# Optimization experiments

Hardware: AMD Instinct MI355X
Metric: run time of the kernel (lower is better)

## Reference

```python
import jax, jax.numpy as jnp
import numpy as np

EPS = 1e-6


def setup_inputs() -> dict:
    key = jax.random.key(0)
    ks = jax.random.split(key, 8)
    B, L, C = 2, 512, 768  # d_model=768, C//3=256
    pairDim = 128
    inp = {
        "x": jax.random.normal(ks[0], (B, L, C), dtype=jnp.float32),
        "ln_w": jnp.ones((C,), jnp.float32),
        "ln_b": jnp.zeros((C,), jnp.float32),
        # torch Linear weights are [out, in]
        "W1": jax.random.normal(ks[1], (256, C // 3), jnp.float32) * (1.0 / np.sqrt(C // 3)),
        "b1": jax.random.normal(ks[2], (256,), jnp.float32) * 0.02,
        "Wa": jax.random.normal(ks[3], (64, 64), jnp.float32) * (1.0 / np.sqrt(64)),
        "ba": jax.random.normal(ks[4], (64,), jnp.float32) * 0.02,
        "W2": jax.random.normal(ks[5], (pairDim, 32), jnp.float32) * (1.0 / np.sqrt(32)),
        "b2": jax.random.normal(ks[6], (pairDim,), jnp.float32) * 0.02,
    }
    return inp


def _layernorm(x, w, b):
    mu = jnp.mean(x, axis=-1, keepdims=True)
    var = jnp.mean(jnp.square(x - mu), axis=-1, keepdims=True)
    return (x - mu) * jax.lax.rsqrt(var + EPS) * w + b


def reference(x, ln_w, ln_b, W1, b1, Wa, ba, W2, b2):
    B, L, C = x.shape
    h = _layernorm(x, ln_w, ln_b)                      # [B,L,C]
    h = h.reshape(B, L, 3, C // 3)                     # [B,L,3,C/3]
    t = (h @ W1.T + b1).reshape(B, L, 3, 32, 8)        # [B,L,3,32,8]
    # outer product t[...,i]*t[...,j] then mean over the 3 chunks (fused)
    mean_out = jnp.einsum('blkci,blkcj->blcij', t, t) / 3.0  # [B,L,32,8,8]
    mean_out = mean_out.reshape(B, L, 32, 64).transpose(0, 2, 1, 3)  # [B,32,L,64]
    mean_trans = jax.nn.gelu(mean_out @ Wa.T + ba, approximate=False)  # [B,32,L,64]
    raw = jnp.einsum('bcld,bcmd->bclm', mean_out, mean_trans)  # [B,32,L,L]
    raw = raw.transpose(0, 2, 3, 1)                    # [B,L,L,32]
    return raw @ W2.T + b2                             # [B,L,L,pairDim]
```

## Files before the change

### kernel.cpp

```cpp
#include <hip/hip_runtime.h>
#include <math.h>


typedef __attribute__((ext_vector_type(8))) _Float16 half8;
typedef __attribute__((ext_vector_type(4))) _Float16 half4;
typedef __attribute__((ext_vector_type(4))) float f32x4;

#define MFMA_F16(a,b,c) __builtin_amdgcn_mfma_f32_16x16x32_f16((a),(b),(c),0,0,0)

static __device__ inline unsigned pack2f16(float a, float b) {
    _Float16 ha = (_Float16)a, hb = (_Float16)b;
    unsigned short ua = __builtin_bit_cast(unsigned short, ha);
    unsigned short ub = __builtin_bit_cast(unsigned short, hb);
    return (unsigned)ua | ((unsigned)ub << 16);
}

static __device__ inline half8 cvt8(float4 u, float4 v) {
    half8 h;
    h[0] = (_Float16)u.x; h[1] = (_Float16)u.y; h[2] = (_Float16)u.z; h[3] = (_Float16)u.w;
    h[4] = (_Float16)v.x; h[5] = (_Float16)v.y; h[6] = (_Float16)v.z; h[7] = (_Float16)v.w;
    return h;
}

static __device__ inline float gelu_fast(float v) {
    float u  = 0.7978845608028654f * (v + 0.044715f * v * v * v);
    float t  = __expf(-2.0f * fabsf(u));
    float th = 1.0f - 2.0f * t / (1.0f + t);
    th = copysignf(th, u);
    return 0.5f * v * (1.0f + th);
}

__global__ __launch_bounds__(256) void k0_pack(const float* __restrict__ W1, _Float16* __restrict__ W1H)
{
    int flat8 = blockIdx.x * 256 + threadIdx.x;
    int j  = flat8 >> 5, i8 = flat8 & 31;
    int nt = j >> 4, lr = j & 15, ks = i8 >> 2, lk = i8 & 3;
    const float4* src = (const float4*)(W1 + (size_t)j * 256 + (size_t)i8 * 8);
    half8 h = cvt8(src[0], src[1]);
    *(half8*)(W1H + (((size_t)(nt * 8 + ks) * 64) + lk * 16 + lr) * 8) = h;
}

__global__ __launch_bounds__(256, 2) void k1_rowstage2(
    const float* __restrict__ x, const float* __restrict__ ln_w, const float* __restrict__ ln_b,
    const _Float16* __restrict__ W1H, const float* __restrict__ b1,
    const float* __restrict__ Wa, const float* __restrict__ ba,
    _Float16* __restrict__ mo_g, _Float16* __restrict__ mt_g)
{
    const int blk = blockIdx.x;
    const int b   = blk >> 8;
    const int l0  = (blk & 255) << 1;
    const int tid = threadIdx.x;
    const int w   = tid >> 6;
    const int lane = tid & 63;
    const int lr  = lane & 15;
    const int lk  = lane >> 4;

    __shared__ _Float16 hs16[16 * 280];
    __shared__ float ts2[2][776];
    __shared__ float mos2[2][2176];

    half8 bfr[32];
    #pragma unroll
    for (int ks = 0; ks < 8; ++ks)
        #pragma unroll
        for (int n = 0; n < 4; ++n)
            bfr[ks * 4 + n] = *(const half8*)(W1H + (((size_t)((w * 4 + n) * 8 + ks) * 64) + lane) * 8);

    half8 waf[2];
    #pragma unroll
    for (int ks = 0; ks < 2; ++ks) {
        const float* wp = Wa + (size_t)(w * 16 + lr) * 64 + ks * 32 + lk * 8;
        waf[ks] = cvt8(*(const float4*)wp, *(const float4*)(wp + 4));
    }
    const float4 baq = *(const float4*)(ba + w * 16 + lk * 4);

    if (w < 2) {
        const float4* xrow = (const float4*)(x + ((size_t)(b * 512 + l0 + w)) * 768);
        float4 xv[3];
        float s1 = 0.f, s2 = 0.f;
        #pragma unroll
        for (int e4 = 0; e4 < 3; ++e4) {
            float4 v = xrow[lane + 64 * e4];
            xv[e4] = v;
            s1 += v.x + v.y + v.z + v.w;
            s2 += v.x * v.x + v.y * v.y + v.z * v.z + v.w * v.w;
        }
        #pragma unroll
        for (int off = 32; off > 0; off >>= 1) {
            s1 += __shfl_xor(s1, off);
            s2 += __shfl_xor(s2, off);
        }
        float mu   = s1 * (1.0f / 768.0f);
        float var  = s2 * (1.0f / 768.0f) - mu * mu;
        float rstd = rsqrtf(var + 1e-6f);
        #pragma unroll
        for (int e4 = 0; e4 < 3; ++e4) {
            float4 lw = ((const float4*)ln_w)[lane + 64 * e4];
            float4 lb = ((const float4*)ln_b)[lane + 64 * e4];
            half4 h4;
            h4[0] = (_Float16)((xv[e4].x - mu) * rstd * lw.x + lb.x);
            h4[1] = (_Float16)((xv[e4].y - mu) * rstd * lw.y + lb.y);
            h4[2] = (_Float16)((xv[e4].z - mu) * rstd * lw.z + lb.z);
            h4[3] = (_Float16)((xv[e4].w - mu) * rstd * lw.w + lb.w);
            *(half4*)&hs16[(w * 3 + e4) * 280 + 4 * lane] = h4;
        }
    }
    __syncthreads();

    {
        f32x4 acc[4] = {};
        #pragma unroll
        for (int ks = 0; ks < 8; ++ks) {
            half8 af = *(const half8*)&hs16[lr * 280 + ks * 32 + lk * 8];
            #pragma unroll
            for (int n = 0; n < 4; ++n)
                acc[n] = MFMA_F16(af, bfr[ks * 4 + n], acc[n]);
        }
        #pragma unroll
        for (int n = 0; n < 4; ++n) {
            int j = (w * 4 + n) * 16 + lr;
            float bb = b1[j];
            #pragma unroll
            for (int jj = 0; jj < 4; ++jj) {
                int m = lk * 4 + jj;
                if (m < 6) {
                    int r = (m >= 3) ? 1 : 0, k = m - r * 3;
                    ts2[r][k * 256 + j] = acc[n][jj] + bb;
                }
            }
        }
    }
    __syncthreads();

    {
        const int c = tid >> 3, i = tid & 7;
        #pragma unroll
        for (int r = 0; r < 2; ++r) {
            float ti0 = ts2[r][c * 8 + i], ti1 = ts2[r][256 + c * 8 + i], ti2 = ts2[r][512 + c * 8 + i];
            float4 a0 = *(const float4*)&ts2[r][c * 8];
            float4 a1 = *(const float4*)&ts2[r][c * 8 + 4];
            float4 b0 = *(const float4*)&ts2[r][256 + c * 8];
            float4 b1v = *(const float4*)&ts2[r][256 + c * 8 + 4];
            float4 d0 = *(const float4*)&ts2[r][512 + c * 8];
            float4 d1 = *(const float4*)&ts2[r][512 + c * 8 + 4];
            float m0 = (ti0 * a0.x + ti1 * b0.x + ti2 * d0.x) * (1.0f / 3.0f);
            float m1 = (ti0 * a0.y + ti1 * b0.y + ti2 * d0.y) * (1.0f / 3.0f);
            float m2 = (ti0 * a0.z + ti1 * b0.z + ti2 * d0.z) * (1.0f / 3.0f);
            float m3 = (ti0 * a0.w + ti1 * b0.w + ti2 * d0.w) * (1.0f / 3.0f);
            float m4 = (ti0 * a1.x + ti1 * b1v.x + ti2 * d1.x) * (1.0f / 3.0f);
            float m5 = (ti0 * a1.y + ti1 * b1v.y + ti2 * d1.y) * (1.0f / 3.0f);
            float m6 = (ti0 * a1.z + ti1 * b1v.z + ti2 * d1.z) * (1.0f / 3.0f);
            float m7 = (ti0 * a1.w + ti1 * b1v.w + ti2 * d1.w) * (1.0f / 3.0f);
            *(float4*)&mos2[r][c * 68 + i * 8]     = make_float4(m0, m1, m2, m3);
            *(float4*)&mos2[r][c * 68 + i * 8 + 4] = make_float4(m4, m5, m6, m7);
            half8 h8;
            h8[0] = (_Float16)m0; h8[1] = (_Float16)m1; h8[2] = (_Float16)m2; h8[3] = (_Float16)m3;
            h8[4] = (_Float16)m4; h8[5] = (_Float16)m5; h8[6] = (_Float16)m6; h8[7] = (_Float16)m7;
            size_t mobase = ((size_t)(b * 32 + c) * 512 + (l0 + r)) * 64 + i * 8;
            *(half8*)(mo_g + mobase) = h8;
        }
    }
    __syncthreads();

    #pragma unroll
    for (int nt2 = 0; nt2 < 4; ++nt2) {
        const int r = nt2 >> 1, ch = nt2 & 1;
        f32x4 acc = { baq.x, baq.y, baq.z, baq.w };
        #pragma unroll
        for (int ks = 0; ks < 2; ++ks) {
            const float* mp = &mos2[r][(ch * 16 + lr) * 68 + ks * 32 + lk * 8];
            half8 mof = cvt8(*(const float4*)mp, *(const float4*)(mp + 4));
            acc = MFMA_F16(waf[ks], mof, acc);
        }
        half4 o;
        #pragma unroll
        for (int j = 0; j < 4; ++j)
            o[j] = (_Float16)gelu_fast(acc[j]);
        *(half4*)(mt_g + ((size_t)(b * 32 + ch * 16 + lr) * 512 + (l0 + r)) * 64 + w * 16 + lk * 4) = o;
    }
}

__global__ __launch_bounds__(256, 2) void k2_mfma(
    const _Float16* __restrict__ mo, const _Float16* __restrict__ mt,
    const float* __restrict__ W2, const float* __restrict__ b2,
    float* __restrict__ out)
{
    __shared__ _Float16 raw16[512 * 40];
    __shared__ float sc[4][2048];

    const int tid  = threadIdx.x;
    const int w    = tid >> 6;
    const int lane = tid & 63;
    const int lr   = lane & 15;
    const int lk   = lane >> 4;

    const int flat = blockIdx.x;
    const int nf   = (flat & 7) * 128 + (flat >> 3);
    const int m0   = (nf & 31) << 4;
    const int l0   = ((nf >> 5) & 15) << 5;
    const int b    = nf >> 9;

    #pragma unroll
    for (int cp = 0; cp < 4; ++cp) {
        const int c0 = w * 8 + cp * 2;
        f32x4 acc[2][2] = {};
        #pragma unroll
        for (int ci = 0; ci < 2; ++ci) {
            const int c = c0 + ci;
            const _Float16* mo_c = mo + (((size_t)(b * 32 + c) * 512) + l0) * 64;
            const _Float16* mt_c = mt + (((size_t)(b * 32 + c) * 512) + m0) * 64;
            #pragma unroll
            for (int ks = 0; ks < 2; ++ks) {
                half8 bfrag = *(const half8*)(mt_c + (size_t)lr * 64 + ks * 32 + lk * 8);
                #pragma unroll
                for (int rh = 0; rh < 2; ++rh) {
                    half8 afrag = *(const half8*)(mo_c + (size_t)(rh * 16 + lr) * 64 + ks * 32 + lk * 8);
                    acc[ci][rh] = MFMA_F16(afrag, bfrag, acc[ci][rh]);
                }
            }
        }
        #pragma unroll
        for (int rh = 0; rh < 2; ++rh) {
            #pragma unroll
            for (int j = 0; j < 4; ++j) {
                int pair = (rh * 16 + lk * 4 + j) * 16 + lr;
                int sw   = (((pair >> 3) & 1) << 3) | (((pair >> 6) & 1) << 4);
                *(unsigned*)&raw16[pair * 40 + (c0 ^ sw)] = pack2f16(acc[0][rh][j], acc[1][rh][j]);
            }
        }
    }

    half8 wfrag[8]; float4 b2q[8];
    #pragma unroll
    for (int c8 = 0; c8 < 8; ++c8) {
        const float* wp = W2 + (size_t)(c8 * 16 + lr) * 32 + lk * 8;
        wfrag[c8] = cvt8(*(const float4*)wp, *(const float4*)(wp + 4));
        b2q[c8]   = *(const float4*)(b2 + c8 * 16 + lk * 4);
    }
    __syncthreads();

    for (int i = 0; i < 8; ++i) {
        const int r  = w * 8 + i;
        const int pr = r * 16 + lr;
        const int swr = (((pr >> 3) & 1) << 3) | (((pr >> 6) & 1) << 4);
        half8 a = *(const half8*)&raw16[pr * 40 + ((lk * 8) ^ swr)];

        #pragma unroll
        for (int c8 = 0; c8 < 8; ++c8) {
            f32x4 d = { b2q[c8].x, b2q[c8].y, b2q[c8].z, b2q[c8].w };
            d = MFMA_F16(wfrag[c8], a, d);
            int chunk = (c8 * 4 + lk) ^ lr;
            *(f32x4*)&sc[w][lr * 128 + chunk * 4] = d;
        }
        float* ob = out + (((size_t)(b * 512 + l0 + r)) * 512 + m0) * 128;
        #pragma unroll
        for (int s = 0; s < 8; ++s) {
            int mm = s * 2 + (lane >> 5);
            int cp = (lane & 31) ^ mm;
            f32x4 v = *(const f32x4*)&sc[w][mm * 128 + cp * 4];
            __builtin_nontemporal_store(v, (f32x4*)(ob + s * 256 + lane * 4));
        }
    }
}

extern "C" void kernel_launch(void* const* d_in, const int* in_sizes, int n_in,
                              void* d_out, int out_size, void* d_ws, size_t ws_size,
                              hipStream_t stream) {
    const float* x    = (const float*)d_in[0];
    const float* ln_w = (const float*)d_in[1];
    const float* ln_b = (const float*)d_in[2];
    const float* W1   = (const float*)d_in[3];
    const float* b1   = (const float*)d_in[4];
    const float* Wa   = (const float*)d_in[5];
    const float* ba   = (const float*)d_in[6];
    const float* W2   = (const float*)d_in[7];
    const float* b2   = (const float*)d_in[8];
    float* out = (float*)d_out;

    _Float16* mo  = (_Float16*)d_ws;
    _Float16* mt  = mo + (size_t)2 * 32 * 512 * 64;
    _Float16* W1H = mt + (size_t)2 * 32 * 512 * 64;

    k0_pack<<<32, 256, 0, stream>>>(W1, W1H);
    k1_rowstage2<<<512, 256, 0, stream>>>(x, ln_w, ln_b, W1H, b1, Wa, ba, mo, mt);
    k2_mfma<<<1024, 256, 0, stream>>>(mo, mt, W2, b2, out);
}
```

Baseline: 75.09 us.

## Make each wave compute its own raw rows across all channels to drop block barrier

```diff
diff --git a/kernel.cpp b/kernel.cpp
--- a/kernel.cpp
+++ b/kernel.cpp
@@ -180,7 +180,7 @@
     }
 }
 
-__global__ __launch_bounds__(256, 2) void k2_mfma(
+__global__ __launch_bounds__(256, 2) void k2_wp(
     const _Float16* __restrict__ mo, const _Float16* __restrict__ mt,
     const float* __restrict__ W2, const float* __restrict__ b2,
     float* __restrict__ out)
@@ -193,6 +193,7 @@
     const int lane = tid & 63;
     const int lr   = lane & 15;
     const int lk   = lane >> 4;
+    const int lw   = lr & 7;
 
     const int flat = blockIdx.x;
     const int nf   = (flat & 7) * 128 + (flat >> 3);
@@ -200,44 +201,40 @@
     const int l0   = ((nf >> 5) & 15) << 5;
     const int b    = nf >> 9;
 
-    #pragma unroll
-    for (int cp = 0; cp < 4; ++cp) {
-        const int c0 = w * 8 + cp * 2;
-        f32x4 acc[2][2] = {};
+    half8 wfrag[8]; float4 b2q[8];
+    #pragma unroll
+    for (int c8 = 0; c8 < 8; ++c8) {
+        const float* wp = W2 + (size_t)(c8 * 16 + lr) * 32 + lk * 8;
+        wfrag[c8] = cvt8(*(const float4*)wp, *(const float4*)(wp + 4));
+        b2q[c8]   = *(const float4*)(b2 + c8 * 16 + lk * 4);
+    }
+
+    #pragma unroll
+    for (int cp = 0; cp < 16; ++cp) {
+        const int c0 = cp * 2;
+        f32x4 acc[2] = {};
         #pragma unroll
         for (int ci = 0; ci < 2; ++ci) {
             const int c = c0 + ci;
-            const _Float16* mo_c = mo + (((size_t)(b * 32 + c) * 512) + l0) * 64;
+            const _Float16* mo_c = mo + (((size_t)(b * 32 + c) * 512) + l0 + w * 8) * 64;
             const _Float16* mt_c = mt + (((size_t)(b * 32 + c) * 512) + m0) * 64;
             #pragma unroll
             for (int ks = 0; ks < 2; ++ks) {
                 half8 bfrag = *(const half8*)(mt_c + (size_t)lr * 64 + ks * 32 + lk * 8);
-                #pragma unroll
-                for (int rh = 0; rh < 2; ++rh) {
-                    half8 afrag = *(const half8*)(mo_c + (size_t)(rh * 16 + lr) * 64 + ks * 32 + lk * 8);
-                    acc[ci][rh] = MFMA_F16(afrag, bfrag, acc[ci][rh]);
-                }
+                half8 afrag = *(const half8*)(mo_c + (size_t)lw * 64 + ks * 32 + lk * 8);
+                acc[ci] = MFMA_F16(afrag, bfrag, acc[ci]);
             }
         }
         #pragma unroll
-        for (int rh = 0; rh < 2; ++rh) {
-            #pragma unroll
-            for (int j = 0; j < 4; ++j) {
-                int pair = (rh * 16 + lk * 4 + j) * 16 + lr;
+        for (int j = 0; j < 4; ++j) {
+            int row = lk * 4 + j;
+            if (row < 8) {
+                int pair = (w * 8 + row) * 16 + lr;
                 int sw   = (((pair >> 3) & 1) << 3) | (((pair >> 6) & 1) << 4);
-                *(unsigned*)&raw16[pair * 40 + (c0 ^ sw)] = pack2f16(acc[0][rh][j], acc[1][rh][j]);
+                *(unsigned*)&raw16[pair * 40 + (c0 ^ sw)] = pack2f16(acc[0][j], acc[1][j]);
             }
         }
     }
-
-    half8 wfrag[8]; float4 b2q[8];
-    #pragma unroll
-    for (int c8 = 0; c8 < 8; ++c8) {
-        const float* wp = W2 + (size_t)(c8 * 16 + lr) * 32 + lk * 8;
-        wfrag[c8] = cvt8(*(const float4*)wp, *(const float4*)(wp + 4));
-        b2q[c8]   = *(const float4*)(b2 + c8 * 16 + lk * 4);
-    }
-    __syncthreads();
 
     for (int i = 0; i < 8; ++i) {
         const int r  = w * 8 + i;
@@ -256,8 +253,8 @@
         #pragma unroll
         for (int s = 0; s < 8; ++s) {
             int mm = s * 2 + (lane >> 5);
-            int cp = (lane & 31) ^ mm;
-            f32x4 v = *(const f32x4*)&sc[w][mm * 128 + cp * 4];
+            int cp2 = (lane & 31) ^ mm;
+            f32x4 v = *(const f32x4*)&sc[w][mm * 128 + cp2 * 4];
             __builtin_nontemporal_store(v, (f32x4*)(ob + s * 256 + lane * 4));
         }
     }
@@ -283,5 +280,5 @@
 
     k0_pack<<<32, 256, 0, stream>>>(W1, W1H);
     k1_rowstage2<<<512, 256, 0, stream>>>(x, ln_w, ln_b, W1H, b1, Wa, ba, mo, mt);
-    k2_mfma<<<1024, 256, 0, stream>>>(mo, mt, W2, b2, out);
-}
+    k2_wp<<<1024, 256, 0, stream>>>(mo, mt, W2, b2, out);
+}
```

New measurement: 121.9 us. +62.3%, slower.
